# Optimization experiments

Measured on AMD Instinct MI355X. Metric: run time of the kernel, lower is better.

The kernel has to match this reference:

```python
import jax, jax.numpy as jnp
import numpy as np

N_NODES = 10000
IN_F = 512
OUT_F = 512
N_EDGES = 160000
GRID_SIZE = 5      # KAN spline grid intervals
SPLINE_ORDER = 3   # cubic B-splines -> GRID_SIZE + SPLINE_ORDER = 8 basis fns per input dim
ALPHA = 0.2        # LeakyReLU negative slope


def _grid():
    # uniform extended grid on [-1, 1], shape [GRID_SIZE + 2*SPLINE_ORDER + 1]
    step = 2.0 / GRID_SIZE
    return jnp.arange(-SPLINE_ORDER, GRID_SIZE + SPLINE_ORDER + 1, dtype=jnp.float32) * step - 1.0


def _b_splines(x, grid):
    # x: [N, in] -> basis: [N, in, GRID_SIZE + SPLINE_ORDER] via Cox-de Boor recursion
    x = x[..., None]  # [N, in, 1]
    bases = ((x >= grid[:-1]) & (x < grid[1:])).astype(x.dtype)  # order-0
    for p in range(1, SPLINE_ORDER + 1):
        left = (x - grid[: -(p + 1)]) / (grid[p:-1] - grid[: -(p + 1)]) * bases[..., :-1]
        right = (grid[p + 1:] - x) / (grid[p + 1:] - grid[1:-p]) * bases[..., 1:]
        bases = left + right
    return bases


def setup_inputs() -> dict:
    key = jax.random.key(0)
    k1, k2, k3, k4, k5, k6 = jax.random.split(key, 6)
    h = jax.random.normal(k1, (N_NODES, IN_F), dtype=jnp.float32)
    edge_index = jax.random.randint(k2, (2, N_EDGES), 0, N_NODES, dtype=jnp.int64)
    xav = float(np.sqrt(2.0 / (IN_F + OUT_F))) * 1.414
    W = jax.random.normal(k3, (IN_F, OUT_F), dtype=jnp.float32) * xav
    a = jax.random.normal(k4, (2 * OUT_F, 1), dtype=jnp.float32) * float(np.sqrt(2.0 / (2 * OUT_F + 1)))
    base_w = jax.random.normal(k5, (OUT_F, IN_F), dtype=jnp.float32) * xav
    n_coef = GRID_SIZE + SPLINE_ORDER
    spline_w = jax.random.normal(k6, (OUT_F, IN_F, n_coef), dtype=jnp.float32) * 0.1
    return {"h": h, "W": W, "a": a, "base_w": base_w, "spline_w": spline_w, "edge_index": edge_index}


def reference(h, W, a, base_w, spline_w, edge_index):
    HW = h @ W  # [N, out]
    row, col = edge_index[0], edge_index[1]
    # a_input @ a == HW_i @ a[:out] + HW_j @ a[out:] (same math, avoids the concat)
    s = HW @ a[:OUT_F, 0]   # [N]
    t = HW @ a[OUT_F:, 0]   # [N]
    e = jax.nn.leaky_relu(s[row] + t[col], negative_slope=ALPHA)  # [E]
    # segment softmax keyed on destination (row)
    m = jax.ops.segment_max(e, row, num_segments=N_NODES)
    ex = jnp.exp(e - m[row])
    den = jax.ops.segment_sum(ex, row, num_segments=N_NODES)
    att = ex / den[row]
    # dropout p=0.6 is identity in eval mode
    # scatter-add aggregation of raw features h[col] (as in the source)
    agg = jax.ops.segment_sum(att[:, None] * h[col], row, num_segments=N_NODES)  # [N, in]
    # KANLayer: silu base path + B-spline path (efficient-KAN formulation)
    grid = _grid()
    basis = _b_splines(agg, grid)  # [N, in, n_coef]
    out = jax.nn.silu(agg) @ base_w.T + jnp.einsum('nip,oip->no', basis, spline_w)
    return out
```

## Files before the change

kernel.cpp:

```cpp
#include <hip/hip_runtime.h>
#include <hip/hip_bf16.h>
#include <math.h>

#define N_NODES 10000
#define IN_F 512
#define OUT_F 512
#define N_EDGES 160000
#define K_SPLINE 4096
#define K_TOTAL 4608
#define NBK 144
#define NBM 628
#define ALPHA 0.2f

typedef __attribute__((ext_vector_type(8))) short short8;
typedef __attribute__((ext_vector_type(4))) float f32x4;
typedef unsigned short ushort_t;
typedef unsigned long long u64;

#define WAITVM(N) asm volatile("s_waitcnt vmcnt(" #N ")" ::: "memory")

__device__ __forceinline__ unsigned bfpair(float a, float b) {
    __hip_bfloat162 h2 = __float22bfloat162_rn(make_float2(a, b));
    return *reinterpret_cast<unsigned*>(&h2);
}
__device__ __forceinline__ float bflo(unsigned u) { return __uint_as_float(u << 16); }
__device__ __forceinline__ float bfhi(unsigned u) { return __uint_as_float(u & 0xffff0000u); }

__device__ __forceinline__ float silu_f(float x) {
    return x / (1.f + __expf(-x));
}

__device__ __forceinline__ uint4 spline_window(float x) {
    float xc = (x + 2.2f) * 2.5f;
    float fc = floorf(xc);
    int c = (int)fc;
    float u = xc - fc;
    float omu = 1.f - u;
    float u2 = u * u, u3 = u2 * u;
    float n0 = (1.f / 6.f) * omu * omu * omu;
    float n1 = 0.5f * u3 - u2 + (2.f / 3.f);
    float n2 = -0.5f * u3 + 0.5f * u2 + 0.5f * u + (1.f / 6.f);
    float n3 = (1.f / 6.f) * u3;
    u64 V = (u64)bfpair(n0, n1) | ((u64)bfpair(n2, n3) << 32);
    int sh = (c - 3) * 16;
    u64 lo, hi;
    if (c < 0 || c > 10)    { lo = 0; hi = 0; }
    else if (sh >= 64)      { lo = 0; hi = V << (sh - 64); }
    else if (sh > 0)        { lo = V << sh; hi = V >> (64 - sh); }
    else if (sh == 0)       { lo = V; hi = 0; }
    else                    { lo = V >> (-sh); hi = 0; }
    uint4 pk;
    pk.x = (unsigned)lo; pk.y = (unsigned)(lo >> 32);
    pk.z = (unsigned)hi; pk.w = (unsigned)(hi >> 32);
    return pk;
}

__global__ void fused1_kernel(const float* __restrict__ W, const float* __restrict__ a,
                              float* __restrict__ wa0, float* __restrict__ wa1,
                              const float* __restrict__ base_w, const float* __restrict__ spline_w,
                              ushort_t* __restrict__ Bt,
                              const float* __restrict__ h, ushort_t* __restrict__ hb,
                              const int* __restrict__ ei, int* __restrict__ deg) {
    int b = blockIdx.x;
    int tid = threadIdx.x;
    if (b < 128) {
        int w = tid >> 6, l = tid & 63;
        int i = b * 4 + w;
        float s0 = 0.f, s1 = 0.f;
        #pragma unroll
        for (int oo = 0; oo < 8; ++oo) {
            int o = l + oo * 64;
            float wv = W[(size_t)i * OUT_F + o];
            s0 += wv * a[o];
            s1 += wv * a[OUT_F + o];
        }
        #pragma unroll
        for (int off = 32; off > 0; off >>= 1) {
            s0 += __shfl_down(s0, off, 64);
            s1 += __shfl_down(s1, off, 64);
        }
        if (l == 0) { wa0[i] = s0; wa1[i] = s1; }
    } else if (b < 1280) {
        int gid = (b - 128) * 256 + tid;
        int o = gid / 576;
        int kb8 = gid - o * 576;
        int k0 = kb8 * 8;
        float4 x0, x1;
        if (k0 < K_SPLINE) {
            const float4* p = (const float4*)(spline_w + (size_t)o * K_SPLINE + k0);
            x0 = p[0]; x1 = p[1];
        } else {
            const float4* p = (const float4*)(base_w + (size_t)o * IN_F + (k0 - K_SPLINE));
            x0 = p[0]; x1 = p[1];
        }
        int frag = (k0 >> 5) * 32 + (o >> 4);
        int lane = ((kb8 & 3) << 4) + (o & 15);
        uint4 pk;
        pk.x = bfpair(x0.x, x0.y);
        pk.y = bfpair(x0.z, x0.w);
        pk.z = bfpair(x1.x, x1.y);
        pk.w = bfpair(x1.z, x1.w);
        *(uint4*)(Bt + ((size_t)frag * 64 + lane) * 8) = pk;
    } else if (b < 3780) {
        int id = (b - 1280) * 256 + tid;
        const float4* p = (const float4*)(h + (size_t)id * 8);
        float4 a0 = p[0], a1 = p[1];
        uint4 pk;
        pk.x = bfpair(a0.x, a0.y);
        pk.y = bfpair(a0.z, a0.w);
        pk.z = bfpair(a1.x, a1.y);
        pk.w = bfpair(a1.z, a1.w);
        *(uint4*)(hb + (size_t)id * 8) = pk;
    } else {
        int k = (b - 3780) * 256 + tid;
        if (k < N_EDGES) atomicAdd(&deg[ei[k]], 1);
    }
}

__global__ void fused2_kernel(const float* __restrict__ h, const float* __restrict__ wa0,
                              const float* __restrict__ wa1,
                              float* __restrict__ s, float* __restrict__ t,
                              const int* __restrict__ deg, int* __restrict__ off,
                              int* __restrict__ cursor) {
    __shared__ int sb[256];
    int b = blockIdx.x;
    int tid = threadIdx.x;
    if (b < 2500) {
        int w = tid >> 6, l = tid & 63;
        int n = b * 4 + w;
        const float4* hp = (const float4*)(h + (size_t)n * IN_F);
        float4 hA = hp[l], hB = hp[l + 64];
        float4 wA0 = ((const float4*)wa0)[l], wB0 = ((const float4*)wa0)[l + 64];
        float4 wA1 = ((const float4*)wa1)[l], wB1 = ((const float4*)wa1)[l + 64];
        float ss = hA.x*wA0.x + hA.y*wA0.y + hA.z*wA0.z + hA.w*wA0.w
                 + hB.x*wB0.x + hB.y*wB0.y + hB.z*wB0.z + hB.w*wB0.w;
        float tt = hA.x*wA1.x + hA.y*wA1.y + hA.z*wA1.z + hA.w*wA1.w
                 + hB.x*wB1.x + hB.y*wB1.y + hB.z*wB1.z + hB.w*wB1.w;
        #pragma unroll
        for (int o = 32; o > 0; o >>= 1) {
            ss += __shfl_down(ss, o, 64);
            tt += __shfl_down(tt, o, 64);
        }
        if (l == 0) { s[n] = ss; t[n] = tt; }
    } else {
        int d[40];
        int tot = 0;
        #pragma unroll
        for (int j = 0; j < 40; ++j) {
            int idx = tid * 40 + j;
            d[j] = (idx < N_NODES) ? deg[idx] : 0;
            tot += d[j];
        }
        sb[tid] = tot;
        __syncthreads();
        for (int sd = 1; sd < 256; sd <<= 1) {
            int v = (tid >= sd) ? sb[tid - sd] : 0;
            __syncthreads();
            sb[tid] += v;
            __syncthreads();
        }
        int run = (tid > 0) ? sb[tid - 1] : 0;
        #pragma unroll
        for (int j = 0; j < 40; ++j) {
            int idx = tid * 40 + j;
            if (idx < N_NODES) { off[idx] = run; cursor[idx] = run; }
            run += d[j];
        }
        if (tid == 255) off[N_NODES] = sb[255];
    }
}

__global__ void fill_kernel(const int* __restrict__ ei, int* __restrict__ cursor,
                            int* __restrict__ csr_col) {
    int k = blockIdx.x * 256 + threadIdx.x;
    if (k < N_EDGES) {
        int r = ei[k];
        int c = ei[N_EDGES + k];
        int p = atomicAdd(&cursor[r], 1);
        csr_col[p] = c;
    }
}

__global__ __launch_bounds__(256) void agg_kernel(
    const ushort_t* __restrict__ hb, const float* __restrict__ s,
    const float* __restrict__ t, const int* __restrict__ off,
    const int* __restrict__ csr, float* __restrict__ agg) {
    int w = threadIdx.x >> 6, l = threadIdx.x & 63;
    int n = blockIdx.x * 4 + w;
    int e0 = off[n], e1 = off[n + 1];
    float sn = s[n];

    float m = -1e30f, den = 0.f;
    for (int k = e0 + l; k < e1; k += 64) {
        float v = sn + t[csr[k]];
        v = (v >= 0.f) ? v : ALPHA * v;
        float mn = fmaxf(m, v);
        den = den * __expf(m - mn) + __expf(v - mn);
        m = mn;
    }
    #pragma unroll
    for (int o = 1; o < 64; o <<= 1) {
        float m2 = __shfl_xor(m, o, 64);
        float d2 = __shfl_xor(den, o, 64);
        float mn = fmaxf(m, m2);
        den = den * __expf(m - mn) + d2 * __expf(m2 - mn);
        m = mn;
    }
    float inv = (den > 0.f) ? 1.f / den : 0.f;

    float acc[8] = {0.f, 0.f, 0.f, 0.f, 0.f, 0.f, 0.f, 0.f};
    const ushort_t* hbl = hb + l * 8;
    for (int base = e0; base < e1; base += 64) {
        int cnt = e1 - base; if (cnt > 64) cnt = 64;
        int c = 0; float att = 0.f;
        if (l < cnt) {
            c = csr[base + l];
            float v = sn + t[c];
            v = (v >= 0.f) ? v : ALPHA * v;
            att = __expf(v - m) * inv;
        }
        #pragma unroll 2
        for (int j = 0; j < cnt; ++j) {
            float aj = __shfl(att, j, 64);
            int cj = __shfl(c, j, 64);
            uint4 u = *(const uint4*)(hbl + (size_t)cj * IN_F);
            acc[0] = fmaf(aj, bflo(u.x), acc[0]);
            acc[1] = fmaf(aj, bfhi(u.x), acc[1]);
            acc[2] = fmaf(aj, bflo(u.y), acc[2]);
            acc[3] = fmaf(aj, bfhi(u.y), acc[3]);
            acc[4] = fmaf(aj, bflo(u.z), acc[4]);
            acc[5] = fmaf(aj, bfhi(u.z), acc[5]);
            acc[6] = fmaf(aj, bflo(u.w), acc[6]);
            acc[7] = fmaf(aj, bfhi(u.w), acc[7]);
        }
    }
    float* arow = agg + (size_t)n * IN_F + l * 8;
    *(float4*)arow       = make_float4(acc[0], acc[1], acc[2], acc[3]);
    *(float4*)(arow + 4) = make_float4(acc[4], acc[5], acc[6], acc[7]);
}

__global__ void expand_kernel(const float* __restrict__ agg, ushort_t* __restrict__ Xf) {
    int id = blockIdx.x * 256 + threadIdx.x;
    int l = id & 63;
    int fid = id >> 6;
    int nb = fid / NBK;
    int kb = fid - nb * NBK;
    int n = nb * 16 + (l & 15);
    uint4 pk = make_uint4(0u, 0u, 0u, 0u);
    if (n < N_NODES) {
        if (kb < 128) {
            int dim = kb * 4 + (l >> 4);
            pk = spline_window(agg[(size_t)n * IN_F + dim]);
        } else {
            const float* ap = agg + (size_t)n * IN_F + (kb - 128) * 32 + (l >> 4) * 8;
            float4 x0 = *(const float4*)ap;
            float4 x1 = *(const float4*)(ap + 4);
            pk.x = bfpair(silu_f(x0.x), silu_f(x0.y));
            pk.y = bfpair(silu_f(x0.z), silu_f(x0.w));
            pk.z = bfpair(silu_f(x1.x), silu_f(x1.y));
            pk.w = bfpair(silu_f(x1.z), silu_f(x1.w));
        }
    }
    *(uint4*)(Xf + (size_t)id * 8) = pk;
}

__global__ __launch_bounds__(256, 2) void kan_gemm2(
    const ushort_t* __restrict__ Xf, const ushort_t* __restrict__ Bt,
    float* __restrict__ out) {
    __shared__ ushort_t A_lds[4][2][4][64][8];

    int d = blockIdx.x;
    int g = d >> 5, r = d & 31;
    int bm = g * 8 + (r & 7), bn = r >> 3;
    if (bm >= 157) return;
    int tid = threadIdx.x, w = tid >> 6, l = tid & 63;
    int wc16 = bn * 8 + w * 2;

    f32x4 acc[4][2];
    #pragma unroll
    for (int m = 0; m < 4; ++m)
        #pragma unroll
        for (int nf = 0; nf < 2; ++nf)
            acc[m][nf] = (f32x4){0.f, 0.f, 0.f, 0.f};

    short8 brA[4], brB[4];

    auto stage = [&](int j, int pb) {
        #pragma unroll
        for (int ks = 0; ks < 2; ++ks) {
            const ushort_t* src = Xf + (((size_t)(bm * 4 + w) * NBK + 2 * j + ks) * 64 + l) * 8;
            __builtin_amdgcn_global_load_lds(
                (const __attribute__((address_space(1))) unsigned int*)src,
                (__attribute__((address_space(3))) unsigned int*)&A_lds[pb][ks][w][0][0],
                16, 0, 0);
        }
    };
    auto loadB = [&](int j, short8 (&b)[4]) {
        int kb = 2 * j;
        #pragma unroll
        for (int ks = 0; ks < 2; ++ks) {
            b[ks * 2 + 0] = *(const short8*)(Bt + ((size_t)((kb + ks) * 32 + wc16)     * 64 + l) * 8);
            b[ks * 2 + 1] = *(const short8*)(Bt + ((size_t)((kb + ks) * 32 + wc16 + 1) * 64 + l) * 8);
        }
    };
    auto compute = [&](int pb, short8 (&b)[4]) {
        __builtin_amdgcn_s_setprio(1);
        #pragma unroll
        for (int ks = 0; ks < 2; ++ks)
            #pragma unroll
            for (int m = 0; m < 4; ++m) {
                short8 af = *(const short8*)&A_lds[pb][ks][m][l][0];
                acc[m][0] = __builtin_amdgcn_mfma_f32_16x16x32_bf16(af, b[ks * 2 + 0], acc[m][0], 0, 0, 0);
                acc[m][1] = __builtin_amdgcn_mfma_f32_16x16x32_bf16(af, b[ks * 2 + 1], acc[m][1], 0, 0, 0);
            }
        __builtin_amdgcn_s_setprio(0);
    };

    stage(0, 0); stage(1, 1); stage(2, 2);
    loadB(0, brA);

    for (int j = 0; j < 70; j += 2) {
        WAITVM(8);
        __builtin_amdgcn_s_barrier();
        __builtin_amdgcn_sched_barrier(0);
        loadB(j + 1, brB);
        stage(j + 3, (j + 3) & 3);
        compute(j & 3, brA);

        WAITVM(8);
        __builtin_amdgcn_s_barrier();
        __builtin_amdgcn_sched_barrier(0);
        loadB(j + 2, brA);
        if (j + 4 < 72) stage(j + 4, (j + 4) & 3);
        compute((j + 1) & 3, brB);
    }
    WAITVM(6);
    __builtin_amdgcn_s_barrier();
    __builtin_amdgcn_sched_barrier(0);
    loadB(71, brB);
    compute(2, brA);
    WAITVM(4);
    __builtin_amdgcn_s_barrier();
    __builtin_amdgcn_sched_barrier(0);
    compute(3, brB);

    #pragma unroll
    for (int m = 0; m < 4; ++m) {
        int r0 = bm * 64 + m * 16 + ((l >> 4) << 2);
        #pragma unroll
        for (int nf = 0; nf < 2; ++nf) {
            int colg = bn * 128 + w * 32 + nf * 16 + (l & 15);
            #pragma unroll
            for (int jr = 0; jr < 4; ++jr) {
                int rr = r0 + jr;
                if (rr < N_NODES) out[(size_t)rr * OUT_F + colg] = acc[m][nf][jr];
            }
        }
    }
}

extern "C" void kernel_launch(void* const* d_in, const int* in_sizes, int n_in,
                              void* d_out, int out_size, void* d_ws, size_t ws_size,
                              hipStream_t stream) {
    const float* h        = (const float*)d_in[0];
    const float* W        = (const float*)d_in[1];
    const float* a        = (const float*)d_in[2];
    const float* base_w   = (const float*)d_in[3];
    const float* spline_w = (const float*)d_in[4];
    const int*   ei       = (const int*)d_in[5];
    float* out = (float*)d_out;

    char* ws = (char*)d_ws;
    size_t cur = 0;
    auto alloc = [&](size_t bytes) -> void* {
        void* p = ws + cur;
        cur += (bytes + 255) & ~(size_t)255;
        return p;
    };
    float* wa0    = (float*)alloc(512 * 4);
    float* wa1    = (float*)alloc(512 * 4);
    float* s      = (float*)alloc(N_NODES * 4);
    float* t      = (float*)alloc(N_NODES * 4);
    int*   deg    = (int*)alloc(N_NODES * 4);
    int*   offp   = (int*)alloc((N_NODES + 1) * 4);
    int*   cursor = (int*)alloc(N_NODES * 4);
    int*   csr    = (int*)alloc(N_EDGES * 4);
    float* agg    = (float*)alloc((size_t)N_NODES * IN_F * 4);
    ushort_t* Bt  = (ushort_t*)alloc((size_t)K_TOTAL * OUT_F * 2);
    ushort_t* hb  = (ushort_t*)alloc((size_t)N_NODES * IN_F * 2);
    ushort_t* Xf  = (ushort_t*)alloc((size_t)NBM * NBK * 64 * 16);
    if (cur > ws_size) return;

    hipMemsetAsync(deg, 0, N_NODES * 4, stream);
    fused1_kernel<<<4405, 256, 0, stream>>>(W, a, wa0, wa1, base_w, spline_w, Bt, h, hb, ei, deg);
    fused2_kernel<<<2501, 256, 0, stream>>>(h, wa0, wa1, s, t, deg, offp, cursor);
    fill_kernel<<<(N_EDGES + 255) / 256, 256, 0, stream>>>(ei, cursor, csr);
    agg_kernel<<<2500, 256, 0, stream>>>(hb, s, t, offp, csr, agg);
    expand_kernel<<<NBM * NBK * 64 / 256, 256, 0, stream>>>(agg, Xf);
    kan_gemm2<<<640, 256, 0, stream>>>(Xf, Bt, out);
}
```

Measured before the change: 170.4 us.

## Replace 4-stage vmcnt pipeline in KAN GEMM with 2-stage double buffer

Rewrites the main loop of the spline/base GEMM so each step covers four k-blocks instead of two, and uses two LDS buffers with plain __syncthreads in place of a four-deep ring with explicit vmcnt waits, sched barriers and setprio. Launch bounds rise to three blocks per SM, and the edge aggregation inner loop is unrolled by four. The aim is to cut per-iteration barrier and wait overhead and to raise occupancy. The cost is shallower prefetch: __syncthreads waits on all outstanding loads, so load latency may be exposed, and the larger B register arrays may pressure registers under the tighter launch bound.

```diff
diff --git a/kernel.cpp b/kernel.cpp
--- a/kernel.cpp
+++ b/kernel.cpp
@@ -16,8 +16,6 @@
 typedef __attribute__((ext_vector_type(4))) float f32x4;
 typedef unsigned short ushort_t;
 typedef unsigned long long u64;
-
-#define WAITVM(N) asm volatile("s_waitcnt vmcnt(" #N ")" ::: "memory")
 
 __device__ __forceinline__ unsigned bfpair(float a, float b) {
     __hip_bfloat162 h2 = __float22bfloat162_rn(make_float2(a, b));
@@ -219,7 +217,7 @@
             v = (v >= 0.f) ? v : ALPHA * v;
             att = __expf(v - m) * inv;
         }
-        #pragma unroll 2
+        #pragma unroll 4
         for (int j = 0; j < cnt; ++j) {
             float aj = __shfl(att, j, 64);
             int cj = __shfl(c, j, 64);
@@ -264,10 +262,10 @@
     *(uint4*)(Xf + (size_t)id * 8) = pk;
 }
 
-__global__ __launch_bounds__(256, 2) void kan_gemm2(
+__global__ __launch_bounds__(256, 3) void kan_gemm2(
     const ushort_t* __restrict__ Xf, const ushort_t* __restrict__ Bt,
     float* __restrict__ out) {
-    __shared__ ushort_t A_lds[4][2][4][64][8];
+    __shared__ ushort_t A_lds[2][4][4][64][8];
 
     int d = blockIdx.x;
     int g = d >> 5, r = d & 31;
@@ -283,66 +281,48 @@
         for (int nf = 0; nf < 2; ++nf)
             acc[m][nf] = (f32x4){0.f, 0.f, 0.f, 0.f};
 
-    short8 brA[4], brB[4];
+    short8 b0[8], b1[8];
 
     auto stage = [&](int j, int pb) {
         #pragma unroll
-        for (int ks = 0; ks < 2; ++ks) {
-            const ushort_t* src = Xf + (((size_t)(bm * 4 + w) * NBK + 2 * j + ks) * 64 + l) * 8;
+        for (int ks = 0; ks < 4; ++ks) {
+            const ushort_t* src = Xf + (((size_t)(bm * 4 + w) * NBK + 4 * j + ks) * 64 + l) * 8;
             __builtin_amdgcn_global_load_lds(
                 (const __attribute__((address_space(1))) unsigned int*)src,
                 (__attribute__((address_space(3))) unsigned int*)&A_lds[pb][ks][w][0][0],
                 16, 0, 0);
         }
     };
-    auto loadB = [&](int j, short8 (&b)[4]) {
-        int kb = 2 * j;
-        #pragma unroll
-        for (int ks = 0; ks < 2; ++ks) {
-            b[ks * 2 + 0] = *(const short8*)(Bt + ((size_t)((kb + ks) * 32 + wc16)     * 64 + l) * 8);
-            b[ks * 2 + 1] = *(const short8*)(Bt + ((size_t)((kb + ks) * 32 + wc16 + 1) * 64 + l) * 8);
+    auto loadB = [&](int j, short8 (&b)[8]) {
+        #pragma unroll
+        for (int ks = 0; ks < 4; ++ks) {
+            int kb = 4 * j + ks;
+            b[ks * 2 + 0] = *(const short8*)(Bt + ((size_t)(kb * 32 + wc16)     * 64 + l) * 8);
+            b[ks * 2 + 1] = *(const short8*)(Bt + ((size_t)(kb * 32 + wc16 + 1) * 64 + l) * 8);
         }
     };
-    auto compute = [&](int pb, short8 (&b)[4]) {
-        __builtin_amdgcn_s_setprio(1);
-        #pragma unroll
-        for (int ks = 0; ks < 2; ++ks)
+    auto compute = [&](int pb, short8 (&b)[8]) {
+        #pragma unroll
+        for (int ks = 0; ks < 4; ++ks)
             #pragma unroll
             for (int m = 0; m < 4; ++m) {
                 short8 af = *(const short8*)&A_lds[pb][ks][m][l][0];
                 acc[m][0] = __builtin_amdgcn_mfma_f32_16x16x32_bf16(af, b[ks * 2 + 0], acc[m][0], 0, 0, 0);
                 acc[m][1] = __builtin_amdgcn_mfma_f32_16x16x32_bf16(af, b[ks * 2 + 1], acc[m][1], 0, 0, 0);
             }
-        __builtin_amdgcn_s_setprio(0);
     };
 
-    stage(0, 0); stage(1, 1); stage(2, 2);
-    loadB(0, brA);
-
-    for (int j = 0; j < 70; j += 2) {
-        WAITVM(8);
-        __builtin_amdgcn_s_barrier();
-        __builtin_amdgcn_sched_barrier(0);
-        loadB(j + 1, brB);
-        stage(j + 3, (j + 3) & 3);
-        compute(j & 3, brA);
-
-        WAITVM(8);
-        __builtin_amdgcn_s_barrier();
-        __builtin_amdgcn_sched_barrier(0);
-        loadB(j + 2, brA);
-        if (j + 4 < 72) stage(j + 4, (j + 4) & 3);
-        compute((j + 1) & 3, brB);
-    }
-    WAITVM(6);
-    __builtin_amdgcn_s_barrier();
-    __builtin_amdgcn_sched_barrier(0);
-    loadB(71, brB);
-    compute(2, brA);
-    WAITVM(4);
-    __builtin_amdgcn_s_barrier();
-    __builtin_amdgcn_sched_barrier(0);
-    compute(3, brB);
+    stage(0, 0);
+    loadB(0, b0);
+    __syncthreads();
+    for (int j = 0; j < 36; j += 2) {
+        if (j + 1 < 36) { stage(j + 1, 1); loadB(j + 1, b1); }
+        compute(0, b0);
+        __syncthreads();
+        if (j + 2 < 36) { stage(j + 2, 0); loadB(j + 2, b0); }
+        compute(1, b1);
+        __syncthreads();
+    }
 
     #pragma unroll
     for (int m = 0; m < 4; ++m) {
```

After: 168.3 us. About the same (-1.3%).
